# Kernel tuning notes

Measured on AMD Instinct MI355X. Metric: run time of the kernel, lower is better.

The kernel has to match this reference:

```python
import jax, jax.numpy as jnp
import numpy as np
from jax import lax

B, PN, NS = 8, 16384, 256
KDIM, HID = 512, 384
HALF = HID // 2
EPS = 1e-5


def setup_inputs() -> dict:
    key = jax.random.key(0)
    ks = jax.random.split(key, 12)
    s = lambda fan: np.float32(1.0 / np.sqrt(fan))
    inp = {
        "p": jax.random.normal(ks[0], (B, PN, 3), jnp.float32),
        "N": NS,
        "patch_feature": jax.random.normal(ks[1], (B, KDIM, 1), jnp.float32),
        # Linear(k_dim, hidden)
        "W_feat": jax.random.normal(ks[2], (KDIM, HID), jnp.float32) * s(KDIM),
        "b_feat": jax.random.normal(ks[3], (HID,), jnp.float32) * s(KDIM),
        # Linear(3, hidden//2)
        "W_coord": jax.random.normal(ks[4], (3, HALF), jnp.float32) * s(3),
        "b_coord": jax.random.normal(ks[5], (HALF,), jnp.float32) * s(3),
        # Conv1d(hidden+hidden//2, hidden, 1) == per-point linear, weight (out,in)
        "W1": jax.random.normal(ks[6], (HID, HID + HALF), jnp.float32) * s(HID + HALF),
        "b1": jax.random.normal(ks[7], (HID,), jnp.float32) * s(HID + HALF),
        "g1": jnp.ones((HID,), jnp.float32),
        "be1": jnp.zeros((HID,), jnp.float32),
        # Conv1d(hidden, hidden, 1)
        "W2": jax.random.normal(ks[8], (HID, HID), jnp.float32) * s(HID),
        "b2": jax.random.normal(ks[9], (HID,), jnp.float32) * s(HID),
        "g2": jnp.ones((HID,), jnp.float32),
        "be2": jnp.zeros((HID,), jnp.float32),
    }
    return inp


def farthest_point_sample(points, k):
    """points: (B, N, C) -> (B, k, C). Deterministic start index 0 per batch."""
    b, n, c = points.shape

    def step(carry, _):
        dist, far = carry
        centroid = jnp.take_along_axis(points, far[:, None, None], axis=1)  # (B,1,C)
        d = jnp.sum((points - centroid) ** 2, axis=-1)                      # (B,N)
        dist = jnp.minimum(dist, d)
        new_far = jnp.argmax(dist, axis=-1)
        return (dist, new_far), far

    init = (jnp.full((b, n), 1e10, points.dtype), jnp.zeros((b,), jnp.int32))
    _, idx = lax.scan(step, init, None, length=k)  # idx: (k, B)
    idx = idx.T                                    # (B, k)
    return jnp.take_along_axis(points, idx[:, :, None], axis=1)  # (B,k,C)


def batchnorm(x, gamma, beta):
    """x: (B, L, C); training-mode BN over (B, L) per channel (biased var)."""
    mean = jnp.mean(x, axis=(0, 1))
    var = jnp.var(x, axis=(0, 1))
    return (x - mean) * lax.rsqrt(var + EPS) * gamma + beta


def reference(p, N, patch_feature, W_feat, b_feat, W_coord, b_coord,
              W1, b1, g1, be1, W2, b2, g2, be2):
    b, pn, _ = p.shape
    global_feat = patch_feature[..., 0] @ W_feat + b_feat          # (B, HID)
    global_feat = jnp.broadcast_to(global_feat[:, None, :], (b, N, HID))
    local_feat = p @ W_coord + b_coord                              # (B, PN, HALF)
    if N != pn:
        local_feat = farthest_point_sample(local_feat, N)           # (B, N, HALF)
    combined = jnp.concatenate([global_feat, local_feat], axis=-1)  # (B, N, HID+HALF)
    h = jnp.einsum("bnc,oc->bno", combined, W1) + b1
    h = jax.nn.relu(batchnorm(h, g1, be1))
    h = jnp.einsum("bnc,oc->bno", h, W2) + b2
    h = jax.nn.relu(batchnorm(h, g2, be2))
    return h  # (B, N, HID)
```

## Files before the change

kernel.cpp:

```cpp
#include <hip/hip_runtime.h>

#define BATCH 8
#define PN    16384
#define NSAMP 256
#define KDIM  512
#define HID   384
#define HALF  192
#define CIN   576
#define ROWS  2048
#define BN_EPS 1e-5f

#define OFF_GF   0
#define OFF_W1T  3072
#define OFF_W2T  224256
#define OFF_IDX  371712
#define OFF_H1   373760
#define OFF_H2   1160192
#define OFF_SUM1 1946624
#define OFF_SQ1  1947008
#define OFF_SUM2 1947392
#define OFF_SQ2  1947776

typedef float v2f __attribute__((ext_vector_type(2)));

__global__ __launch_bounds__(1024) void k_main(const float* p, const float* Wc,
                                               const float* pf, const float* Wf,
                                               const float* bfe, const float* W1,
                                               const float* W2, float* ws) {
  __shared__ float s[KDIM];
  __shared__ float Msh[6];
  __shared__ __align__(16) float redv[2][16];
  __shared__ int widx[2];
  int blk = blockIdx.x, t = threadIdx.x;

  if (blk >= 8) {
    if (blk < 16) {
      for (int sI = (blk - 8) * 1024 + t; sI < HID * CIN; sI += 8192) {
        int o = sI / CIN, c = sI % CIN;
        ws[OFF_W1T + c * HID + o] = W1[sI];
      }
    } else if (blk < 24) {
      for (int sI = (blk - 16) * 1024 + t; sI < HID * HID; sI += 8192) {
        int o = sI / HID, c = sI % HID;
        ws[OFF_W2T + c * HID + o] = W2[sI];
      }
    } else if (blk < 32) {
      int b = blk - 24;
      if (t < KDIM) s[t] = pf[b * KDIM + t];
      __syncthreads();
      if (t < HID) {
        float acc = bfe[t];
        for (int k = 0; k < KDIM; k++) acc = fmaf(s[k], Wf[k * HID + t], acc);
        ws[OFF_GF + b * HID + t] = acc;
      }
    } else {
      for (int i = t; i < 1536; i += 1024) ws[OFF_SUM1 + i] = 0.f;
    }
    return;
  }

  int b = blk;
  int* idx_out = (int*)(ws + OFF_IDX);

  if (t < 64) {
    double g0 = 0, g1 = 0, g2 = 0, g3 = 0, g4 = 0, g5 = 0;
    for (int k = t; k < HALF; k += 64) {
      double w0 = (double)Wc[k];
      double w1 = (double)Wc[HALF + k];
      double w2 = (double)Wc[2 * HALF + k];
      g0 += w0 * w0; g1 += w0 * w1; g2 += w0 * w2;
      g3 += w1 * w1; g4 += w1 * w2; g5 += w2 * w2;
    }
    for (int off = 32; off; off >>= 1) {
      g0 += __shfl_down(g0, off, 64); g1 += __shfl_down(g1, off, 64);
      g2 += __shfl_down(g2, off, 64); g3 += __shfl_down(g3, off, 64);
      g4 += __shfl_down(g4, off, 64); g5 += __shfl_down(g5, off, 64);
    }
    if (t == 0) {
      double l00 = sqrt(g0);
      double l10 = g1 / l00, l20 = g2 / l00;
      double l11 = sqrt(g3 - l10 * l10);
      double l21 = (g4 - l10 * l20) / l11;
      double l22 = sqrt(g5 - l20 * l20 - l21 * l21);
      Msh[0] = (float)l00; Msh[1] = (float)l10; Msh[2] = (float)l20;
      Msh[3] = (float)l11; Msh[4] = (float)l21; Msh[5] = (float)l22;
    }
  }
  __syncthreads();
  float m00 = Msh[0], m10 = Msh[1], m20 = Msh[2];
  float m11 = Msh[3], m21 = Msh[4], m22 = Msh[5];

  const float* pb = p + b * PN * 3;
  v2f qx[8], qy[8], qz[8], dist[8];
#pragma unroll
  for (int j = 0; j < 8; j++) {
    int i0 = ((2 * j) << 10) + t;
    int i1 = i0 + 1024;
    float x0 = pb[i0 * 3], y0 = pb[i0 * 3 + 1], z0 = pb[i0 * 3 + 2];
    float x1 = pb[i1 * 3], y1 = pb[i1 * 3 + 1], z1 = pb[i1 * 3 + 2];
    qx[j] = (v2f){fmaf(m00, x0, fmaf(m10, y0, m20 * z0)),
                  fmaf(m00, x1, fmaf(m10, y1, m20 * z1))};
    qy[j] = (v2f){fmaf(m11, y0, m21 * z0), fmaf(m11, y1, m21 * z1)};
    qz[j] = (v2f){m22 * z0, m22 * z1};
    dist[j] = (v2f){1e10f, 1e10f};
  }

  int far = 0, par = 0;
  for (int k = 0; k < NSAMP; k++) {
    if (t == 0) {
      idx_out[b * NSAMP + k] = far;
      widx[par] = 0x7fffffff;
    }
    float x = pb[far * 3], y = pb[far * 3 + 1], z = pb[far * 3 + 2];
    float cx = fmaf(m00, x, fmaf(m10, y, m20 * z));
    float cy = fmaf(m11, y, m21 * z);
    float cz = m22 * z;
    v2f cxv = (v2f){cx, cx}, cyv = (v2f){cy, cy}, czv = (v2f){cz, cz};
#pragma unroll
    for (int j = 0; j < 8; j++) {
      v2f dx = qx[j] - cxv, dy = qy[j] - cyv, dz = qz[j] - czv;
      v2f d = __builtin_elementwise_fma(
          dx, dx, __builtin_elementwise_fma(dy, dy, dz * dz));
      dist[j] = __builtin_elementwise_min(dist[j], d);
    }
    float a0 = fmaxf(dist[0].x, dist[0].y);
    float a1 = fmaxf(dist[1].x, dist[1].y);
    float a2 = fmaxf(dist[2].x, dist[2].y);
    float a3 = fmaxf(dist[3].x, dist[3].y);
    float a4 = fmaxf(dist[4].x, dist[4].y);
    float a5 = fmaxf(dist[5].x, dist[5].y);
    float a6 = fmaxf(dist[6].x, dist[6].y);
    float a7 = fmaxf(dist[7].x, dist[7].y);
    float b0 = fmaxf(fmaxf(a0, a1), a2);
    float b1 = fmaxf(fmaxf(a3, a4), a5);
    float tmax = fmaxf(fmaxf(b0, b1), fmaxf(a6, a7));
    float m = tmax;
#pragma unroll
    for (int off = 32; off; off >>= 1) m = fmaxf(m, __shfl_xor(m, off, 64));
    if ((t & 63) == 0) redv[par][t >> 6] = m;
    __syncthreads();
    float4 r0 = *(const float4*)&redv[par][0];
    float4 r1 = *(const float4*)&redv[par][4];
    float4 r2 = *(const float4*)&redv[par][8];
    float4 r3 = *(const float4*)&redv[par][12];
    float g01 = fmaxf(fmaxf(r0.x, r0.y), r0.z);
    float g02 = fmaxf(fmaxf(r0.w, r1.x), r1.y);
    float g03 = fmaxf(fmaxf(r1.z, r1.w), r2.x);
    float g04 = fmaxf(fmaxf(r2.y, r2.z), r2.w);
    float g05 = fmaxf(fmaxf(r3.x, r3.y), r3.z);
    float gmax = fmaxf(fmaxf(fmaxf(g01, g02), g03),
                       fmaxf(fmaxf(g04, g05), r3.w));
    if (tmax == gmax) {
      int mi = 0x7fffffff;
#pragma unroll
      for (int j = 0; j < 8; j++) {
        if (dist[j].x == gmax) mi = min(mi, ((2 * j) << 10) + t);
        if (dist[j].y == gmax) mi = min(mi, ((2 * j + 1) << 10) + t);
      }
      atomicMin(&widx[par], mi);
    }
    __syncthreads();
    far = widx[par];
    par ^= 1;
  }
}

__global__ __launch_bounds__(384) void k_gemm1(const float* p,
                                               const float* Wc,
                                               const float* bc,
                                               const float* b1,
                                               float* ws) {
  __shared__ __align__(16) float ct[CIN * 8];
  int t = threadIdx.x;
  int row0 = blockIdx.x * 8;
  const int* fidx = (const int*)(ws + OFF_IDX);
  for (int sI = t; sI < 8 * CIN; sI += 384) {
    int r = sI / CIN, c = sI % CIN;
    int row = row0 + r, b = row >> 8;
    float val;
    if (c < HID) {
      val = ws[OFF_GF + b * HID + c];
    } else {
      int co = c - HID;
      int i = fidx[row];
      const float* pp = p + (b * PN + i) * 3;
      val = bc[co];
      val = fmaf(pp[0], Wc[co], val);
      val = fmaf(pp[1], Wc[HALF + co], val);
      val = fmaf(pp[2], Wc[2 * HALF + co], val);
    }
    ct[c * 8 + r] = val;
  }
  __syncthreads();
  const float* w1t = ws + OFF_W1T;
  float acc[8] = {0.f, 0.f, 0.f, 0.f, 0.f, 0.f, 0.f, 0.f};
  for (int c = 0; c < CIN; c++) {
    float w = w1t[c * HID + t];
    float4 a0 = *(const float4*)(ct + c * 8);
    float4 a1 = *(const float4*)(ct + c * 8 + 4);
    acc[0] = fmaf(a0.x, w, acc[0]); acc[1] = fmaf(a0.y, w, acc[1]);
    acc[2] = fmaf(a0.z, w, acc[2]); acc[3] = fmaf(a0.w, w, acc[3]);
    acc[4] = fmaf(a1.x, w, acc[4]); acc[5] = fmaf(a1.y, w, acc[5]);
    acc[6] = fmaf(a1.z, w, acc[6]); acc[7] = fmaf(a1.w, w, acc[7]);
  }
  float bias = b1[t];
  float sv = 0.f, sq = 0.f;
#pragma unroll
  for (int r = 0; r < 8; r++) {
    float v = acc[r] + bias;
    ws[OFF_H1 + (row0 + r) * HID + t] = v;
    sv += v; sq = fmaf(v, v, sq);
  }
  atomicAdd(&ws[OFF_SUM1 + t], sv);
  atomicAdd(&ws[OFF_SQ1 + t], sq);
}

__global__ __launch_bounds__(384) void k_gemm2(const float* b2,
                                               const float* g1,
                                               const float* be1,
                                               float* ws) {
  __shared__ __align__(16) float ht[HID * 8];
  __shared__ float sc1s[HID], sh1s[HID];
  int t = threadIdx.x;
  int row0 = blockIdx.x * 8;
  {
    float m = ws[OFF_SUM1 + t] * (1.f / ROWS);
    float v = ws[OFF_SQ1 + t] * (1.f / ROWS) - m * m;
    float inv = 1.f / sqrtf(v + BN_EPS);
    float sc = inv * g1[t];
    sc1s[t] = sc;
    sh1s[t] = be1[t] - m * sc;
  }
  __syncthreads();
  for (int sI = t; sI < 8 * HID; sI += 384) {
    int r = sI / HID, c = sI % HID;
    float x = fmaf(ws[OFF_H1 + (row0 + r) * HID + c], sc1s[c], sh1s[c]);
    ht[c * 8 + r] = fmaxf(x, 0.f);
  }
  __syncthreads();
  const float* w2t = ws + OFF_W2T;
  float acc[8] = {0.f, 0.f, 0.f, 0.f, 0.f, 0.f, 0.f, 0.f};
  for (int c = 0; c < HID; c++) {
    float w = w2t[c * HID + t];
    float4 a0 = *(const float4*)(ht + c * 8);
    float4 a1 = *(const float4*)(ht + c * 8 + 4);
    acc[0] = fmaf(a0.x, w, acc[0]); acc[1] = fmaf(a0.y, w, acc[1]);
    acc[2] = fmaf(a0.z, w, acc[2]); acc[3] = fmaf(a0.w, w, acc[3]);
    acc[4] = fmaf(a1.x, w, acc[4]); acc[5] = fmaf(a1.y, w, acc[5]);
    acc[6] = fmaf(a1.z, w, acc[6]); acc[7] = fmaf(a1.w, w, acc[7]);
  }
  float bias = b2[t];
  float sv = 0.f, sq = 0.f;
#pragma unroll
  for (int r = 0; r < 8; r++) {
    float v = acc[r] + bias;
    ws[OFF_H2 + (row0 + r) * HID + t] = v;
    sv += v; sq = fmaf(v, v, sq);
  }
  atomicAdd(&ws[OFF_SUM2 + t], sv);
  atomicAdd(&ws[OFF_SQ2 + t], sq);
}

__global__ __launch_bounds__(256) void k_out(const float* ws, const float* g2,
                                             const float* be2, float* out) {
  int gid = blockIdx.x * 256 + threadIdx.x;
  int i = gid * 4;
  int c = i % HID;
  float4 h  = *(const float4*)(ws + OFF_H2 + i);
  float4 s2 = *(const float4*)(ws + OFF_SUM2 + c);
  float4 q2 = *(const float4*)(ws + OFF_SQ2 + c);
  float4 gv = *(const float4*)(g2 + c);
  float4 bv = *(const float4*)(be2 + c);
  float4 r;
#define BN2(comp) {                                                  \
    float m  = s2.comp * (1.f / ROWS);                               \
    float v  = q2.comp * (1.f / ROWS) - m * m;                       \
    float sc = (1.f / sqrtf(v + BN_EPS)) * gv.comp;                  \
    float sh = bv.comp - m * sc;                                     \
    r.comp = fmaxf(fmaf(h.comp, sc, sh), 0.f); }
  BN2(x) BN2(y) BN2(z) BN2(w)
#undef BN2
  ((float4*)out)[gid] = r;
}

extern "C" void kernel_launch(void* const* d_in, const int* in_sizes, int n_in,
                              void* d_out, int out_size, void* d_ws, size_t ws_size,
                              hipStream_t stream) {
  const float* p   = (const float*)d_in[0];
  const float* pf  = (const float*)d_in[2];
  const float* Wf  = (const float*)d_in[3];
  const float* bfe = (const float*)d_in[4];
  const float* Wc  = (const float*)d_in[5];
  const float* bc  = (const float*)d_in[6];
  const float* W1  = (const float*)d_in[7];
  const float* b1  = (const float*)d_in[8];
  const float* g1  = (const float*)d_in[9];
  const float* be1 = (const float*)d_in[10];
  const float* W2  = (const float*)d_in[11];
  const float* b2  = (const float*)d_in[12];
  const float* g2  = (const float*)d_in[13];
  const float* be2 = (const float*)d_in[14];
  float* ws = (float*)d_ws;

  hipLaunchKernelGGL(k_main,  dim3(33),  dim3(1024), 0, stream,
                     p, Wc, pf, Wf, bfe, W1, W2, ws);
  hipLaunchKernelGGL(k_gemm1, dim3(256), dim3(384), 0, stream, p, Wc, bc, b1, ws);
  hipLaunchKernelGGL(k_gemm2, dim3(256), dim3(384), 0, stream, b2, g1, be1, ws);
  hipLaunchKernelGGL(k_out,   dim3(768), dim3(256), 0, stream,
                     ws, g2, be2, (float*)d_out);
}
```

Before: 524.6 us.

## Cache winner coords in LDS, use DPP wave reduce and packed f32 asm in FPS

Threads that win the argmax now write their candidate index and transformed coordinates into a small LDS table. The next iteration reads the centroid from that table and avoids a dependent global load of the chosen point, falling back to the load only when the index is not in the table. The wave-level max uses DPP row operations instead of shuffles, and the distance update uses inline-asm packed f32 ops. The table adds bookkeeping (an atomicAdd plus up to 8 slots) and a small chance of falling back to the global load.

```diff
diff --git a/kernel.cpp b/kernel.cpp
--- a/kernel.cpp
+++ b/kernel.cpp
@@ -23,6 +23,27 @@
 
 typedef float v2f __attribute__((ext_vector_type(2)));
 
+__device__ __forceinline__ v2f pk_sub(v2f a, v2f b) {
+  v2f d;
+  asm("v_pk_add_f32 %0, %1, %2 neg_lo:[0,1] neg_hi:[0,1]"
+      : "=v"(d) : "v"(a), "v"(b));
+  return d;
+}
+__device__ __forceinline__ v2f pk_mul(v2f a, v2f b) {
+  v2f d;
+  asm("v_pk_mul_f32 %0, %1, %2" : "=v"(d) : "v"(a), "v"(b));
+  return d;
+}
+__device__ __forceinline__ v2f pk_fma(v2f a, v2f b, v2f c) {
+  v2f d;
+  asm("v_pk_fma_f32 %0, %1, %2, %3" : "=v"(d) : "v"(a), "v"(b), "v"(c));
+  return d;
+}
+
+#define DPP_MAX(v, ctrl)                                                   \
+  v = fmaxf(v, __int_as_float(__builtin_amdgcn_update_dpp(                 \
+          0, __float_as_int(v), (ctrl), 0xf, 0xf, true)))
+
 __global__ __launch_bounds__(1024) void k_main(const float* p, const float* Wc,
                                                const float* pf, const float* Wf,
                                                const float* bfe, const float* W1,
@@ -30,7 +51,9 @@
   __shared__ float s[KDIM];
   __shared__ float Msh[6];
   __shared__ __align__(16) float redv[2][16];
-  __shared__ int widx[2];
+  __shared__ int widx[2], ncl[2];
+  __shared__ int ci[2][8];
+  __shared__ float cxs[2][8], cys[2][8], czs[2][8];
   int blk = blockIdx.x, t = threadIdx.x;
 
   if (blk >= 8) {
@@ -105,23 +128,49 @@
     dist[j] = (v2f){1e10f, 1e10f};
   }
 
-  int far = 0, par = 0;
+  if (t == 0) {
+    widx[1] = 0; ncl[1] = 1; ci[1][0] = 0;
+    cxs[1][0] = qx[0].x; cys[1][0] = qy[0].x; czs[1][0] = qz[0].x;
+    widx[0] = 0x7fffffff; ncl[0] = 0;
+  }
+  __syncthreads();
+
+  int par = 0;
   for (int k = 0; k < NSAMP; k++) {
+    int qb = par ^ 1;
+    int far = widx[qb];
+    int n   = ncl[qb];
+    float cx = cxs[qb][0], cy = cys[qb][0], cz = czs[qb][0];
+    int c0  = ci[qb][0];
+    if (c0 != far) {
+      bool found = false;
+      int nn = n < 8 ? n : 8;
+      for (int i2 = 1; i2 < nn; i2++)
+        if (ci[qb][i2] == far) {
+          cx = cxs[qb][i2]; cy = cys[qb][i2]; cz = czs[qb][i2]; found = true;
+        }
+      if (!found) {
+        float x = pb[far * 3], y = pb[far * 3 + 1], z = pb[far * 3 + 2];
+        cx = fmaf(m00, x, fmaf(m10, y, m20 * z));
+        cy = fmaf(m11, y, m21 * z);
+        cz = m22 * z;
+      }
+    }
     if (t == 0) {
       idx_out[b * NSAMP + k] = far;
       widx[par] = 0x7fffffff;
-    }
-    float x = pb[far * 3], y = pb[far * 3 + 1], z = pb[far * 3 + 2];
-    float cx = fmaf(m00, x, fmaf(m10, y, m20 * z));
-    float cy = fmaf(m11, y, m21 * z);
-    float cz = m22 * z;
+      ncl[par] = 0;
+    }
+
     v2f cxv = (v2f){cx, cx}, cyv = (v2f){cy, cy}, czv = (v2f){cz, cz};
 #pragma unroll
     for (int j = 0; j < 8; j++) {
-      v2f dx = qx[j] - cxv, dy = qy[j] - cyv, dz = qz[j] - czv;
-      v2f d = __builtin_elementwise_fma(
-          dx, dx, __builtin_elementwise_fma(dy, dy, dz * dz));
-      dist[j] = __builtin_elementwise_min(dist[j], d);
+      v2f dx = pk_sub(qx[j], cxv);
+      v2f dy = pk_sub(qy[j], cyv);
+      v2f dz = pk_sub(qz[j], czv);
+      v2f d  = pk_fma(dx, dx, pk_fma(dy, dy, pk_mul(dz, dz)));
+      dist[j].x = fminf(dist[j].x, d.x);
+      dist[j].y = fminf(dist[j].y, d.y);
     }
     float a0 = fmaxf(dist[0].x, dist[0].y);
     float a1 = fmaxf(dist[1].x, dist[1].y);
@@ -134,10 +183,14 @@
     float b0 = fmaxf(fmaxf(a0, a1), a2);
     float b1 = fmaxf(fmaxf(a3, a4), a5);
     float tmax = fmaxf(fmaxf(b0, b1), fmaxf(a6, a7));
-    float m = tmax;
-#pragma unroll
-    for (int off = 32; off; off >>= 1) m = fmaxf(m, __shfl_xor(m, off, 64));
-    if ((t & 63) == 0) redv[par][t >> 6] = m;
+    float wv = tmax;
+    DPP_MAX(wv, 0x111);
+    DPP_MAX(wv, 0x112);
+    DPP_MAX(wv, 0x114);
+    DPP_MAX(wv, 0x118);
+    DPP_MAX(wv, 0x142);
+    DPP_MAX(wv, 0x143);
+    if ((t & 63) == 63) redv[par][t >> 6] = wv;
     __syncthreads();
     float4 r0 = *(const float4*)&redv[par][0];
     float4 r1 = *(const float4*)&redv[par][4];
@@ -151,16 +204,24 @@
     float gmax = fmaxf(fmaxf(fmaxf(g01, g02), g03),
                        fmaxf(fmaxf(g04, g05), r3.w));
     if (tmax == gmax) {
-      int mi = 0x7fffffff;
+      int mi = 0x7fffffff; float wx = 0.f, wy = 0.f, wz = 0.f;
 #pragma unroll
       for (int j = 0; j < 8; j++) {
-        if (dist[j].x == gmax) mi = min(mi, ((2 * j) << 10) + t);
-        if (dist[j].y == gmax) mi = min(mi, ((2 * j + 1) << 10) + t);
+        if (dist[j].x == gmax && mi == 0x7fffffff) {
+          mi = ((2 * j) << 10) + t; wx = qx[j].x; wy = qy[j].x; wz = qz[j].x;
+        }
+        if (dist[j].y == gmax && mi == 0x7fffffff) {
+          mi = ((2 * j + 1) << 10) + t; wx = qx[j].y; wy = qy[j].y; wz = qz[j].y;
+        }
+      }
+      int pos = atomicAdd(&ncl[par], 1);
+      if (pos < 8) {
+        ci[par][pos] = mi;
+        cxs[par][pos] = wx; cys[par][pos] = wy; czs[par][pos] = wz;
       }
       atomicMin(&widx[par], mi);
     }
     __syncthreads();
-    far = widx[par];
     par ^= 1;
   }
 }
```

Result: slower. 594.3 us (+13.3%).
